# Performance work log

Hardware: AMD Instinct MI355X
Metric: run time of the kernel (lower is better)

Reference implementation:

```python
import jax, jax.numpy as jnp
import numpy as np
from math import pi

N_TRAJS, N_RES, N_BINS = 20, 300, 34
DIST_BIN_CENTRES = jnp.asarray(np.array([3.75 + 0.5 * i for i in range(N_BINS)], dtype=np.float32))
SIG = 1.25            # gauss_sigma
K_CB_DIST = 150.0
K_HB_DIST = 5.0
K_HB_GEN = 0.0
K_ANG_HB_GEN = 0.0
W_VIOL_MIN = 3.0      # weight_violate_min
EXP_MIN = 1.0         # pairwise_exponent_min
EXP_MAX = 0.75        # pairwise_exponent_max
HB_CUTOFF = 6.0       # hb_cutoff_gen
CUTOFF = 40.0         # pairwise_force_cutoff


def _norm(d):
    # safe euclidean norm over last axis (avoids NaN grad at exactly 0)
    return jnp.sqrt(jnp.maximum((d * d).sum(axis=-1), 1e-12))


def _safe_pow(x, p):
    pos = x > 0
    return jnp.where(pos, jnp.where(pos, x, 1.0) ** p, 0.0)


def _angle_forces(ba, bc, k, close, true_ang):
    ba_n = _norm(ba)
    bc_n = _norm(bc)
    cosang = jnp.clip((ba * bc).sum(-1) / jnp.clip(ba_n * bc_n, 0.1, 100.0), -1.0 + 1e-6, 1.0 - 1e-6)
    forces = k * close * (jnp.arccos(cosang) - true_ang)
    cr = jnp.cross(ba, bc)
    fa_vec = jnp.cross(-ba, cr)
    fc_vec = jnp.cross(bc, cr)
    fa = forces[..., None] * fa_vec / jnp.maximum(_norm(fa_vec), 0.1)[..., None]
    fc = forces[..., None] * fc_vec / jnp.maximum(_norm(fc_vec), 0.1)[..., None]
    fb = -fa - fc
    return fa, fb, fc


def setup_inputs() -> dict:
    key = jax.random.key(0)
    ks = jax.random.split(key, 9)
    B, R = N_TRAJS, N_RES
    base = jax.random.uniform(ks[0], (B, R, 3), dtype=jnp.float32) * 30.0
    def off(k):
        return base + jax.random.normal(k, (B, R, 3), dtype=jnp.float32)
    coords_N = off(ks[1]); coords_C = off(ks[2]); coords_O = off(ks[3])
    coords_CB = off(ks[4]); coords_H = off(ks[5])
    gaussian_weights = jax.random.normal(ks[6], (R, R, N_BINS), dtype=jnp.float32)
    hb_dists_min = 1.5 + 1.5 * jax.random.uniform(ks[7], (R, R), dtype=jnp.float32)
    hb_dists_max = hb_dists_min + 1.0 + 2.0 * jax.random.uniform(ks[8], (R, R), dtype=jnp.float32)
    return {"coords_N": coords_N, "coords_C": coords_C, "coords_O": coords_O,
            "coords_CB": coords_CB, "coords_H": coords_H,
            "gaussian_weights": gaussian_weights,
            "hb_dists_min": hb_dists_min, "hb_dists_max": hb_dists_max}


def reference(coords_N, coords_C, coords_O, coords_CB, coords_H,
              gaussian_weights, hb_dists_min, hb_dists_max):
    B, R, _ = coords_CB.shape
    idx = jnp.arange(R)
    # mask excluding |i-j| <= 2 (self and near-diagonal), as in the torch diag_mask
    diag_mask = (jnp.abs(idx[:, None] - idx[None, :]) > 2).astype(jnp.float32)[None]

    # --- CB distogram gaussian pairwise forces ---
    diffs_cb = coords_CB[:, None, :, :] - coords_CB[:, :, None, :]   # [B,i,j,3] = cb_j - cb_i
    dists_cb = jnp.clip(_norm(diffs_cb), 0.1, CUTOFF)                 # [B,i,j]
    norm_cb = diffs_cb / dists_cb[..., None]
    dfm = dists_cb[..., None] - DIST_BIN_CENTRES                      # [B,i,j,K]
    cb_e = gaussian_weights[None] * jnp.exp(-0.5 * (dfm / SIG) ** 2) / SIG
    f_cb = (-dfm / (SIG * SIG) * cb_e).sum(axis=3)                    # [B,i,j]
    pair_cb = -f_cb[..., None] * K_CB_DIST * norm_cb
    accs_CB = pair_cb.sum(axis=1)

    # --- H..O hydrogen-bond min/max distance restraints ---
    diffs_ho = coords_O[:, None, :, :] - coords_H[:, :, None, :]      # [B,i,j,3] = o_j - h_i
    dists_ho = jnp.clip(_norm(diffs_ho), 0.1, CUTOFF)
    norm_ho = diffs_ho / dists_ho[..., None]
    v_min = jnp.maximum(hb_dists_min[None] - dists_ho, 0.0)
    v_max = jnp.maximum(dists_ho - hb_dists_max[None], 0.0)
    close = (dists_ho < HB_CUTOFF).astype(jnp.float32) * diag_mask
    v_max_gen = close * jnp.maximum(dists_ho - HB_CUTOFF, 0.0)
    f_min = W_VIOL_MIN * K_HB_DIST * _safe_pow(v_min, EXP_MIN)
    f_max = K_HB_DIST * _safe_pow(v_max, EXP_MAX) + K_HB_GEN * _safe_pow(v_max_gen, EXP_MAX)
    pair_hb = (f_min - f_max)[..., None] * norm_ho
    accs_H = -pair_hb.sum(axis=2)
    accs_O = pair_hb.sum(axis=1)

    # --- O-H-N angle term (k_ang_hb_gen = 0, kept for fidelity) ---
    diffs_hn = (coords_N - coords_H)[:, :, None, :]                   # [B,i,1,3], broadcast over j
    fa, fb, fc = _angle_forces(diffs_ho, diffs_hn, K_ANG_HB_GEN, close, pi)
    accs_O = accs_O + fa.sum(axis=1)
    accs_H = accs_H + fb.sum(axis=2)
    accs_N = fc.sum(axis=2)

    # --- C-O-H angle term ---
    diffs_oc = (coords_C - coords_O)[:, :, None, :]                   # [B,i,1,3]
    fa2, fb2, fc2 = _angle_forces(diffs_oc, -diffs_ho, K_ANG_HB_GEN, close, pi)
    accs_C = fa2.sum(axis=2)
    accs_O = accs_O + fb2.sum(axis=1)
    accs_H = accs_H + fc2.sum(axis=2)

    return (accs_N, accs_C, accs_O, accs_CB, accs_H)
```

## Files before the change

kernel.cpp:

```cpp
#include <hip/hip_runtime.h>

#define NRES  300
#define NTRJ  20
#define NBINS 34
#define PLANE (NTRJ * NRES * 3)
#define TILEF (64 * NBINS)
#define TILE4 (TILEF / 4)
#define NHP   20

#define EXP2F(x) __builtin_exp2f(x)
#define LOG2F(x) __builtin_log2f(x)

__device__ __forceinline__ float g16sum(float v) {
#pragma unroll
  for (int m = 1; m < 16; m <<= 1) v += __shfl_xor(v, m, 64);
  return v;
}

template <int IC, bool PART>
__global__ __launch_bounds__(256)
void force_fused(const float* __restrict__ cO, const float* __restrict__ cCB,
                 const float* __restrict__ cH, const float* __restrict__ gw,
                 const float* __restrict__ hmin, const float* __restrict__ hmax,
                 float* __restrict__ out, float* __restrict__ part) {
  constexpr int NCH = NRES / IC;
  __shared__ float wlds[2][TILEF];
  __shared__ float sCB[NTRJ * IC * 3];
  __shared__ float sHH[NTRJ * IC * 3];

  const int tid  = threadIdx.x;
  const int wv   = tid >> 6;
  const int lane = tid & 63;
  const int bsub = lane >> 4;
  const int jsub = lane & 15;
  const int jt   = blockIdx.x % 5;
  const int ch   = blockIdx.x / 5;
  const int i0   = ch * IC;
  const int j    = jt * 64 + wv * 16 + jsub;
  const bool jv  = (j < NRES);
  const int jc   = jv ? j : NRES - 1;
  const int F4   = (jt == 4) ? ((NRES - 256) * NBINS) / 4 : TILE4;

  for (int e = tid; e < NTRJ * IC * 3; e += 256) {
    const int b = e / (IC * 3), r = e % (IC * 3);
    sCB[e] = cCB[((b * NRES) + i0 + r / 3) * 3 + (r % 3)];
    sHH[e] = cH [((b * NRES) + i0 + r / 3) * 3 + (r % 3)];
  }

  float pjx[5], pjy[5], pjz[5], pox[5], poy[5], poz[5];
  float acx[5] = {}, acy[5] = {}, acz[5] = {};
  float aox[5] = {}, aoy[5] = {}, aoz[5] = {};
#pragma unroll
  for (int q = 0; q < 5; ++q) {
    const int b = bsub * 5 + q;
    const float* p = cCB + ((size_t)(b * NRES + jc)) * 3;
    pjx[q] = p[0]; pjy[q] = p[1]; pjz[q] = p[2];
    const float* o = cO + ((size_t)(b * NRES + jc)) * 3;
    pox[q] = o[0]; poy[q] = o[1]; poz[q] = o[2];
  }

  float4 r4[3];
  {
    const float4* src = (const float4*)(gw + ((size_t)i0 * NRES + jt * 64) * NBINS);
#pragma unroll
    for (int u = 0; u < 3; ++u) {
      const int e = tid + u * 256;
      r4[u] = (e < F4) ? src[e] : make_float4(0.f, 0.f, 0.f, 0.f);
    }
  }

  int p = 0;
  for (int ii = 0; ii < IC; ++ii) {
    const int i = i0 + ii;
    float4* dst = (float4*)wlds[p];
#pragma unroll
    for (int u = 0; u < 3; ++u) {
      const int e = tid + u * 256;
      if (e < TILE4) dst[e] = r4[u];
    }
    __syncthreads();
    if (ii + 1 < IC) {
      const float4* src =
          (const float4*)(gw + ((size_t)(i + 1) * NRES + jt * 64) * NBINS);
#pragma unroll
      for (int u = 0; u < 3; ++u) {
        const int e = tid + u * 256;
        r4[u] = (e < F4) ? src[e] : make_float4(0.f, 0.f, 0.f, 0.f);
      }
    }

    float w[36];
    const float2* p2 = (const float2*)(wlds[p] + (wv * 16 + jsub) * NBINS);
#pragma unroll
    for (int k = 0; k < 17; ++k) { float2 v = p2[k]; w[2*k] = v.x; w[2*k+1] = v.y; }
    w[34] = 0.f; w[35] = 0.f;

    const float hmn = hmin[i * NRES + jc];
    const float hmx = hmax[i * NRES + jc];

#pragma unroll
    for (int q = 0; q < 5; ++q) {
      const int b = bsub * 5 + q;
      const float* pi = &sCB[(b * IC + ii) * 3];
      const float* ph = &sHH[(b * IC + ii) * 3];

      float dx = pjx[q] - pi[0], dy = pjy[q] - pi[1], dz = pjz[q] - pi[2];
      float d2 = fmaf(dx, dx, fmaf(dy, dy, dz * dz));
      d2 = fminf(fmaxf(d2, 0.01f), 1600.0f);
      float rinv = __frsqrt_rn(d2);
      float d    = d2 * rinv;
      float dA = d - 3.75f, dB = d - 9.75f, dC = d - 15.75f;
      float gA = EXP2F(-0.46166241f * dA * dA);
      float mA = EXP2F(fmaf(0.46166241f, dA, -0.11541560f));
      float gB = EXP2F(-0.46166241f * dB * dB);
      float mB = EXP2F(fmaf(0.46166241f, dB, -0.11541560f));
      float gC = EXP2F(-0.46166241f * dC * dC);
      float mC = EXP2F(fmaf(0.46166241f, dC, -0.11541560f));
      float s0 = 0.f, s1 = 0.f, s2 = 0.f;
#pragma unroll
      for (int k = 0; k < 12; ++k) {
        s0 = fmaf(w[k]      * dA, gA, s0); gA *= mA; mA *= 0.85214379f; dA -= 0.5f;
        s1 = fmaf(w[k + 12] * dB, gB, s1); gB *= mB; mB *= 0.85214379f; dB -= 0.5f;
        s2 = fmaf(w[k + 24] * dC, gC, s2); gC *= mC; mC *= 0.85214379f; dC -= 0.5f;
      }
      float cf = 76.8f * ((s0 + s1) + s2) * rinv;
      acx[q] = fmaf(cf, dx, acx[q]);
      acy[q] = fmaf(cf, dy, acy[q]);
      acz[q] = fmaf(cf, dz, acz[q]);

      float ex = pox[q] - ph[0], ey = poy[q] - ph[1], ez = poz[q] - ph[2];
      float e2 = fmaf(ex, ex, fmaf(ey, ey, ez * ez));
      e2 = fminf(fmaxf(e2, 0.01f), 1600.0f);
      float rh = __frsqrt_rn(e2);
      float dh = e2 * rh;
      float vmin = fmaxf(hmn - dh, 0.0f);
      float vmax = fmaxf(dh - hmx, 0.0f);
      float fmn = 15.0f * vmin;
      float fmx = (vmax > 0.0f) ? 5.0f * EXP2F(0.75f * LOG2F(vmax)) : 0.0f;
      float ff = (fmn - fmx) * rh;
      float qx = ff * ex, qy = ff * ey, qz = ff * ez;
      aox[q] += qx; aoy[q] += qy; aoz[q] += qz;

      float sx = g16sum(jv ? qx : 0.f);
      float sy = g16sum(jv ? qy : 0.f);
      float sz = g16sum(jv ? qz : 0.f);
      if (jsub == 0) {
        if constexpr (PART) {
          float* hp = part + ((size_t)(2 * NCH + jt * 4 + wv)) * PLANE +
                      ((size_t)b * NRES + i) * 3;
          hp[0] = -sx; hp[1] = -sy; hp[2] = -sz;
        } else {
          atomicAdd(&out[4 * PLANE + (b * NRES + i) * 3 + 0], -sx);
          atomicAdd(&out[4 * PLANE + (b * NRES + i) * 3 + 1], -sy);
          atomicAdd(&out[4 * PLANE + (b * NRES + i) * 3 + 2], -sz);
        }
      }
    }
    p ^= 1;
  }

  if (jv) {
    if constexpr (PART) {
      float* pc  = part + (size_t)ch * PLANE;
      float* po2 = part + (size_t)(NCH + ch) * PLANE;
#pragma unroll
      for (int q = 0; q < 5; ++q) {
        const int base = ((bsub * 5 + q) * NRES + j) * 3;
        pc[base + 0]  = acx[q]; pc[base + 1]  = acy[q]; pc[base + 2]  = acz[q];
        po2[base + 0] = aox[q]; po2[base + 1] = aoy[q]; po2[base + 2] = aoz[q];
      }
    } else {
#pragma unroll
      for (int q = 0; q < 5; ++q) {
        const int base = ((bsub * 5 + q) * NRES + j) * 3;
        atomicAdd(&out[3 * PLANE + base + 0], acx[q]);
        atomicAdd(&out[3 * PLANE + base + 1], acy[q]);
        atomicAdd(&out[3 * PLANE + base + 2], acz[q]);
        atomicAdd(&out[2 * PLANE + base + 0], aox[q]);
        atomicAdd(&out[2 * PLANE + base + 1], aoy[q]);
        atomicAdd(&out[2 * PLANE + base + 2], aoz[q]);
      }
    }
  }
}

template <int NCH>
__global__ __launch_bounds__(256)
void reduce_all(const float* __restrict__ part, float* __restrict__ out) {
  const int t = blockIdx.x * 256 + threadIdx.x;
  if (t >= PLANE) return;
  const float* pc = part + t;
  const float* po = part + (size_t)NCH * PLANE + t;
  const float* ph = part + (size_t)2 * NCH * PLANE + t;
  float scb = 0.f, so = 0.f, sh = 0.f;
#pragma unroll 5
  for (int c = 0; c < NCH; ++c) {
    scb += pc[(size_t)c * PLANE];
    so  += po[(size_t)c * PLANE];
  }
#pragma unroll
  for (int c = 0; c < NHP; ++c) sh += ph[(size_t)c * PLANE];
  out[0 * PLANE + t] = 0.f;
  out[1 * PLANE + t] = 0.f;
  out[2 * PLANE + t] = so;
  out[3 * PLANE + t] = scb;
  out[4 * PLANE + t] = sh;
}

extern "C" void kernel_launch(void* const* d_in, const int* in_sizes, int n_in,
                              void* d_out, int out_size, void* d_ws, size_t ws_size,
                              hipStream_t stream) {
  const float* cO  = (const float*)d_in[2];
  const float* cCB = (const float*)d_in[3];
  const float* cH  = (const float*)d_in[4];
  const float* gw  = (const float*)d_in[5];
  const float* hmn = (const float*)d_in[6];
  const float* hmx = (const float*)d_in[7];
  float* out  = (float*)d_out;
  float* part = (float*)d_ws;

  const size_t plane_b = (size_t)PLANE * sizeof(float);
  const int nred = (PLANE + 255) / 256;

  if (ws_size >= (2 * 150 + NHP) * plane_b) {
    force_fused<2, true><<<dim3(5 * 150), dim3(256), 0, stream>>>(
        cO, cCB, cH, gw, hmn, hmx, out, part);
    reduce_all<150><<<dim3(nred), dim3(256), 0, stream>>>(part, out);
  } else if (ws_size >= (2 * 75 + NHP) * plane_b) {
    force_fused<4, true><<<dim3(5 * 75), dim3(256), 0, stream>>>(
        cO, cCB, cH, gw, hmn, hmx, out, part);
    reduce_all<75><<<dim3(nred), dim3(256), 0, stream>>>(part, out);
  } else {
    (void)hipMemsetAsync(out, 0, (size_t)out_size * sizeof(float), stream);
    force_fused<4, false><<<dim3(5 * 75), dim3(256), 0, stream>>>(
        cO, cCB, cH, gw, hmn, hmx, out, nullptr);
  }
}
```

Measured before the change: 49.36 us.

## Use per-wave LDS weight staging and split the reduction into parallel segments

Each wave now stages only its own 16 rows of gaussian weights into a private LDS slice. This removes the block-wide __syncthreads in the inner i loop and the double-buffer toggle. The reduction kernel is split into 7 segments per output element that are accumulated with atomics into an output zeroed by a memset, which raises parallelism in the memory-bound reduce. The cost is an extra memset launch and atomic traffic. There is also a possible hazard: a wave overwrites its LDS slice on the next iteration with no barrier, though the reads within a wave are ordered.

```diff
diff --git a/kernel.cpp b/kernel.cpp
--- a/kernel.cpp
+++ b/kernel.cpp
@@ -4,9 +4,12 @@
 #define NTRJ  20
 #define NBINS 34
 #define PLANE (NTRJ * NRES * 3)
-#define TILEF (64 * NBINS)
-#define TILE4 (TILEF / 4)
+#define IC    2
+#define NCH   150
 #define NHP   20
+#define WROW  544
+#define WF2   272
+#define NRED  ((PLANE + 255) / 256)
 
 #define EXP2F(x) __builtin_exp2f(x)
 #define LOG2F(x) __builtin_log2f(x)
@@ -17,14 +20,13 @@
   return v;
 }
 
-template <int IC, bool PART>
+template <bool PART>
 __global__ __launch_bounds__(256)
 void force_fused(const float* __restrict__ cO, const float* __restrict__ cCB,
                  const float* __restrict__ cH, const float* __restrict__ gw,
                  const float* __restrict__ hmin, const float* __restrict__ hmax,
                  float* __restrict__ out, float* __restrict__ part) {
-  constexpr int NCH = NRES / IC;
-  __shared__ float wlds[2][TILEF];
+  __shared__ float wbuf[4][WROW];
   __shared__ float sCB[NTRJ * IC * 3];
   __shared__ float sHH[NTRJ * IC * 3];
 
@@ -36,16 +38,19 @@
   const int jt   = blockIdx.x % 5;
   const int ch   = blockIdx.x / 5;
   const int i0   = ch * IC;
-  const int j    = jt * 64 + wv * 16 + jsub;
+  const int j0w  = jt * 64 + wv * 16;
+  const int j    = j0w + jsub;
   const bool jv  = (j < NRES);
   const int jc   = jv ? j : NRES - 1;
-  const int F4   = (jt == 4) ? ((NRES - 256) * NBINS) / 4 : TILE4;
+  const int nrow = min(16, max(0, NRES - j0w));
+  const int E2   = nrow * 17;
 
   for (int e = tid; e < NTRJ * IC * 3; e += 256) {
     const int b = e / (IC * 3), r = e % (IC * 3);
     sCB[e] = cCB[((b * NRES) + i0 + r / 3) * 3 + (r % 3)];
     sHH[e] = cH [((b * NRES) + i0 + r / 3) * 3 + (r % 3)];
   }
+  __syncthreads();
 
   float pjx[5], pjy[5], pjz[5], pox[5], poy[5], poz[5];
   float acx[5] = {}, acy[5] = {}, acz[5] = {};
@@ -59,38 +64,36 @@
     pox[q] = o[0]; poy[q] = o[1]; poz[q] = o[2];
   }
 
-  float4 r4[3];
+  float2 r2[5];
   {
-    const float4* src = (const float4*)(gw + ((size_t)i0 * NRES + jt * 64) * NBINS);
-#pragma unroll
-    for (int u = 0; u < 3; ++u) {
-      const int e = tid + u * 256;
-      r4[u] = (e < F4) ? src[e] : make_float4(0.f, 0.f, 0.f, 0.f);
-    }
-  }
-
-  int p = 0;
+    const float2* src = (const float2*)gw + ((size_t)i0 * NRES + j0w) * 17;
+#pragma unroll
+    for (int u = 0; u < 5; ++u) {
+      const int e = lane + u * 64;
+      r2[u] = (e < E2) ? src[e] : make_float2(0.f, 0.f);
+    }
+  }
+
+  float2* wd = (float2*)&wbuf[wv][0];
   for (int ii = 0; ii < IC; ++ii) {
     const int i = i0 + ii;
-    float4* dst = (float4*)wlds[p];
-#pragma unroll
-    for (int u = 0; u < 3; ++u) {
-      const int e = tid + u * 256;
-      if (e < TILE4) dst[e] = r4[u];
-    }
-    __syncthreads();
+#pragma unroll
+    for (int u = 0; u < 5; ++u) {
+      const int e = lane + u * 64;
+      if (e < WF2) wd[e] = r2[u];
+    }
     if (ii + 1 < IC) {
-      const float4* src =
-          (const float4*)(gw + ((size_t)(i + 1) * NRES + jt * 64) * NBINS);
-#pragma unroll
-      for (int u = 0; u < 3; ++u) {
-        const int e = tid + u * 256;
-        r4[u] = (e < F4) ? src[e] : make_float4(0.f, 0.f, 0.f, 0.f);
+      const float2* src =
+          (const float2*)gw + ((size_t)(i + 1) * NRES + j0w) * 17;
+#pragma unroll
+      for (int u = 0; u < 5; ++u) {
+        const int e = lane + u * 64;
+        r2[u] = (e < E2) ? src[e] : make_float2(0.f, 0.f);
       }
     }
 
     float w[36];
-    const float2* p2 = (const float2*)(wlds[p] + (wv * 16 + jsub) * NBINS);
+    const float2* p2 = (const float2*)&wbuf[wv][jsub * NBINS];
 #pragma unroll
     for (int k = 0; k < 17; ++k) { float2 v = p2[k]; w[2*k] = v.x; w[2*k+1] = v.y; }
     w[34] = 0.f; w[35] = 0.f;
@@ -156,7 +159,6 @@
         }
       }
     }
-    p ^= 1;
   }
 
   if (jv) {
@@ -184,27 +186,28 @@
   }
 }
 
-template <int NCH>
 __global__ __launch_bounds__(256)
-void reduce_all(const float* __restrict__ part, float* __restrict__ out) {
-  const int t = blockIdx.x * 256 + threadIdx.x;
+void reduce_seg(const float* __restrict__ part, float* __restrict__ out) {
+  const int seg  = blockIdx.x / NRED;
+  const int tblk = blockIdx.x % NRED;
+  const int t    = tblk * 256 + threadIdx.x;
   if (t >= PLANE) return;
-  const float* pc = part + t;
-  const float* po = part + (size_t)NCH * PLANE + t;
-  const float* ph = part + (size_t)2 * NCH * PLANE + t;
-  float scb = 0.f, so = 0.f, sh = 0.f;
-#pragma unroll 5
-  for (int c = 0; c < NCH; ++c) {
-    scb += pc[(size_t)c * PLANE];
-    so  += po[(size_t)c * PLANE];
-  }
-#pragma unroll
-  for (int c = 0; c < NHP; ++c) sh += ph[(size_t)c * PLANE];
-  out[0 * PLANE + t] = 0.f;
-  out[1 * PLANE + t] = 0.f;
-  out[2 * PLANE + t] = so;
-  out[3 * PLANE + t] = scb;
-  out[4 * PLANE + t] = sh;
+
+  int c0, cnt;
+  float* dst;
+  if (seg < 3)      { c0 = seg * 50;             cnt = 50; dst = out + 3 * PLANE; }
+  else if (seg < 6) { c0 = NCH + (seg - 3) * 50; cnt = 50; dst = out + 2 * PLANE; }
+  else              { c0 = 2 * NCH;              cnt = 20; dst = out + 4 * PLANE; }
+
+  const float* p = part + t + (size_t)c0 * PLANE;
+  float s[10] = {};
+  for (int c = 0; c < cnt; c += 10) {
+#pragma unroll
+    for (int u = 0; u < 10; ++u) s[u] += p[(size_t)(c + u) * PLANE];
+  }
+  float tot = ((s[0] + s[1]) + (s[2] + s[3])) + ((s[4] + s[5]) + (s[6] + s[7])) +
+              (s[8] + s[9]);
+  atomicAdd(&dst[t], tot);
 }
 
 extern "C" void kernel_launch(void* const* d_in, const int* in_sizes, int n_in,
@@ -219,20 +222,16 @@
   float* out  = (float*)d_out;
   float* part = (float*)d_ws;
 
-  const size_t plane_b = (size_t)PLANE * sizeof(float);
-  const int nred = (PLANE + 255) / 256;
-
-  if (ws_size >= (2 * 150 + NHP) * plane_b) {
-    force_fused<2, true><<<dim3(5 * 150), dim3(256), 0, stream>>>(
+  const size_t need = (size_t)(2 * NCH + NHP) * PLANE * sizeof(float);
+
+  (void)hipMemsetAsync(out, 0, (size_t)out_size * sizeof(float), stream);
+
+  if (ws_size >= need) {
+    force_fused<true><<<dim3(5 * NCH), dim3(256), 0, stream>>>(
         cO, cCB, cH, gw, hmn, hmx, out, part);
-    reduce_all<150><<<dim3(nred), dim3(256), 0, stream>>>(part, out);
-  } else if (ws_size >= (2 * 75 + NHP) * plane_b) {
-    force_fused<4, true><<<dim3(5 * 75), dim3(256), 0, stream>>>(
-        cO, cCB, cH, gw, hmn, hmx, out, part);
-    reduce_all<75><<<dim3(nred), dim3(256), 0, stream>>>(part, out);
+    reduce_seg<<<dim3(7 * NRED), dim3(256), 0, stream>>>(part, out);
   } else {
-    (void)hipMemsetAsync(out, 0, (size_t)out_size * sizeof(float), stream);
-    force_fused<4, false><<<dim3(5 * 75), dim3(256), 0, stream>>>(
+    force_fused<false><<<dim3(5 * NCH), dim3(256), 0, stream>>>(
         cO, cCB, cH, gw, hmn, hmx, out, nullptr);
   }
 }
```

New measurement: 39.79 us. -19.4%, faster.
